# Optimization experiments

Hardware: AMD Instinct MI355X
Metric: run time of the kernel (lower is better)

Reference implementation:

```python
import jax, jax.numpy as jnp
import numpy as np

N, F, O, S, B, E = 100000, 128, 128, 4, 2, 3200000

def setup_inputs() -> dict:
    key = jax.random.key(0)
    k1, k2, k3, k4, k5, k6 = jax.random.split(key, 6)
    features = jax.random.normal(k1, (N, F), dtype=jnp.float32)
    # xavier-ish scale for weights
    W = jax.random.normal(k2, (B, F, O), dtype=jnp.float32) * (1.0 / np.sqrt(F))
    W_comp = jax.random.normal(k3, (S, B), dtype=jnp.float32)
    edge_rows = jax.random.randint(k4, (S, E), 0, N, dtype=jnp.int32)
    edge_cols = jax.random.randint(k5, (S, E), 0, N, dtype=jnp.int32)
    edge_vals = jax.random.uniform(k6, (S, E), dtype=jnp.float32)
    return {"features": features, "W": W, "W_comp": W_comp,
            "edge_rows": edge_rows, "edge_cols": edge_cols, "edge_vals": edge_vals}

def reference(features, W, W_comp, edge_rows, edge_cols, edge_vals):
    # Basis decomposition: V[s] = sum_b W_comp[s,b] * W[b]   -> [S, F, O]
    V = jnp.einsum('sb,bfo->sfo', W_comp, W)
    # supports[s] = features @ V[s]                            -> [S, N, O]
    supports = jnp.einsum('nf,sfo->sno', features, V)
    num_nodes = features.shape[0]
    def agg(sup, rows, cols, vals):
        # sparse A @ sup: gather source rows, scale by edge val, scatter-add to dest
        msgs = sup[cols] * vals[:, None]          # [E, O]
        return jax.ops.segment_sum(msgs, rows, num_segments=num_nodes)
    outs = jax.vmap(agg)(supports, edge_rows, edge_cols, edge_vals)  # [S, N, O]
    return jnp.tanh(outs.sum(axis=0))
```

## Files before the change

kernel.cpp:

```cpp
#include <hip/hip_runtime.h>
#include <hip/hip_bf16.h>
#include <hip/hip_fp16.h>

#define NN 100000
#define FF 128
#define OO 128
#define SS 4
#define BBASES 2
#define EE 3200000
#define TOTE (SS * EE)
#define BROWS 32
#define NBUK 3125
#define NCOARSE 98
#define SCAP 5120
#define RBLOCKS 512
#define P2PARTS 8

typedef unsigned int uintx2 __attribute__((ext_vector_type(2)));
typedef float floatx4 __attribute__((ext_vector_type(4)));

static __device__ __forceinline__ float2 h2_to_f2(unsigned int u) {
  __half2 h = *reinterpret_cast<__half2*>(&u);
  return __half22float2(h);
}


__global__ __launch_bounds__(256) void histB_kernel(
    const int* __restrict__ rows, unsigned int* __restrict__ bhist) {
  __shared__ unsigned int lh[NBUK];
  for (int i = threadIdx.x; i < NBUK; i += 256) lh[i] = 0;
  __syncthreads();
  const int stride = gridDim.x * 256;
  for (int i = blockIdx.x * 256 + threadIdx.x; i < TOTE; i += stride)
    atomicAdd(&lh[((unsigned)rows[i]) >> 5], 1u);
  __syncthreads();
  for (int i = threadIdx.x; i < NBUK; i += 256) {
    unsigned int c = lh[i];
    if (c) atomicAdd(&bhist[i], c);
  }
}

__global__ __launch_bounds__(256) void scanB_kernel(
    const unsigned int* __restrict__ bhist, unsigned int* __restrict__ bstart,
    unsigned int* __restrict__ fcur, unsigned int* __restrict__ ccur) {
  __shared__ unsigned int sums[256];
  const int C = (NBUK + 255) / 256;
  const int t = threadIdx.x;
  unsigned int s = 0;
  for (int j = 0; j < C; ++j) {
    int i = t * C + j;
    if (i < NBUK) s += bhist[i];
  }
  sums[t] = s;
  __syncthreads();
  for (int off = 1; off < 256; off <<= 1) {
    unsigned int v = (t >= off) ? sums[t - off] : 0u;
    __syncthreads();
    sums[t] += v;
    __syncthreads();
  }
  unsigned int base = (t == 0) ? 0u : sums[t - 1];
  for (int j = 0; j < C; ++j) {
    int i = t * C + j;
    if (i < NBUK) {
      unsigned int h = bhist[i];
      bstart[i] = base;
      fcur[i] = base;
      base += h;
    }
  }
  if (t == 255) bstart[NBUK] = base;
  __syncthreads();
  if (t < NCOARSE) ccur[t] = bstart[t * 32];
}

__global__ __launch_bounds__(256) void part1_kernel(
    const int* __restrict__ rows, const int* __restrict__ cols,
    const float* __restrict__ vals, const float* __restrict__ Wc,
    unsigned int* __restrict__ ccur, uintx2* __restrict__ recsA) {
  __shared__ unsigned int lcnt[NCOARSE];
  __shared__ unsigned int lbase[NCOARSE];
  const float c00 = Wc[0], c01 = Wc[1], c10 = Wc[2], c11 = Wc[3];
  const float c20 = Wc[4], c21 = Wc[5], c30 = Wc[6], c31 = Wc[7];
  const int C = (TOTE + RBLOCKS - 1) / RBLOCKS;
  const int start = blockIdx.x * C;
  const int end = min(start + C, TOTE);
  const int tid = threadIdx.x;
  if (tid < NCOARSE) lcnt[tid] = 0;
  __syncthreads();
  for (int i = start + tid; i < end; i += 256)
    atomicAdd(&lcnt[((unsigned)rows[i]) >> 10], 1u);
  __syncthreads();
  if (tid < NCOARSE) {
    unsigned int c = lcnt[tid];
    lbase[tid] = c ? atomicAdd(&ccur[tid], c) : 0u;
    lcnt[tid] = 0;
  }
  __syncthreads();
  for (int i = start + tid; i < end; i += 256) {
    unsigned int r = (unsigned)rows[i];
    int bk = r >> 10;
    unsigned int p = lbase[bk] + atomicAdd(&lcnt[bk], 1u);
    unsigned int s = (unsigned)(i / EE);
    float val = vals[i];
    float w0 = (s == 0) ? c00 : (s == 1) ? c10 : (s == 2) ? c20 : c30;
    float w1 = (s == 0) ? c01 : (s == 1) ? c11 : (s == 2) ? c21 : c31;
    __half2 hv = __floats2half2_rn(val * w0, val * w1);
    uintx2 rec;
    rec.x = ((unsigned)cols[i]) | ((r & 31u) << 17) | (((r >> 5) & 31u) << 22);
    rec.y = *reinterpret_cast<unsigned int*>(&hv);
    recsA[p] = rec;
  }
}

__global__ __launch_bounds__(256) void part2_kernel(
    const uintx2* __restrict__ recsA, const unsigned int* __restrict__ bstart,
    unsigned int* __restrict__ fcur, uintx2* __restrict__ recsB) {
  __shared__ unsigned int lcnt[32];
  __shared__ unsigned int lbase[32];
  const int c = blockIdx.x >> 3;
  const int p = blockIdx.x & (P2PARTS - 1);
  const int f0 = c * 32;
  const int f1 = min(f0 + 32, NBUK);
  const unsigned int beg = bstart[f0];
  const unsigned int endc = bstart[f1];
  const unsigned int len = endc - beg;
  const unsigned int chunk = (len + P2PARTS - 1) / P2PARTS;
  const unsigned int s0 = beg + (unsigned)p * chunk;
  const unsigned int s1 = min(s0 + chunk, endc);
  const int tid = threadIdx.x;
  if (tid < 32) lcnt[tid] = 0;
  __syncthreads();
  for (unsigned int i = s0 + tid; i < s1; i += 256)
    atomicAdd(&lcnt[(recsA[i].x >> 22) & 31u], 1u);
  __syncthreads();
  if (tid < 32) {
    unsigned int cnt = lcnt[tid];
    lbase[tid] = (cnt && f0 + tid < NBUK) ? atomicAdd(&fcur[f0 + tid], cnt) : 0u;
    lcnt[tid] = 0;
  }
  __syncthreads();
  for (unsigned int i = s0 + tid; i < s1; i += 256) {
    uintx2 r = recsA[i];
    unsigned int j = (r.x >> 22) & 31u;
    unsigned int pos = lbase[j] + atomicAdd(&lcnt[j], 1u);
    recsB[pos] = r;
  }
}

#define RBLOCKSB 256
__global__ __launch_bounds__(1024) void partitionB_kernel(
    const int* __restrict__ rows, const int* __restrict__ cols,
    const float* __restrict__ vals, const float* __restrict__ Wc,
    unsigned int* __restrict__ fcur, uintx2* __restrict__ recs) {
  __shared__ unsigned int lcnt[NBUK];
  __shared__ unsigned int lbase[NBUK];
  const float c00 = Wc[0], c01 = Wc[1], c10 = Wc[2], c11 = Wc[3];
  const float c20 = Wc[4], c21 = Wc[5], c30 = Wc[6], c31 = Wc[7];
  const int C = (TOTE + RBLOCKSB - 1) / RBLOCKSB;
  const int start = blockIdx.x * C;
  const int end = min(start + C, TOTE);
  const int tid = threadIdx.x;
  for (int i = tid; i < NBUK; i += 1024) lcnt[i] = 0;
  __syncthreads();
  for (int i = start + tid; i < end; i += 1024)
    atomicAdd(&lcnt[((unsigned)rows[i]) >> 5], 1u);
  __syncthreads();
  for (int i = tid; i < NBUK; i += 1024) {
    unsigned int c = lcnt[i];
    if (c) lbase[i] = atomicAdd(&fcur[i], c);
    lcnt[i] = 0;
  }
  __syncthreads();
  for (int i = start + tid; i < end; i += 1024) {
    unsigned int r = (unsigned)rows[i];
    int bk = r >> 5;
    unsigned int p = lbase[bk] + atomicAdd(&lcnt[bk], 1u);
    unsigned int s = (unsigned)(i / EE);
    float val = vals[i];
    float w0 = (s == 0) ? c00 : (s == 1) ? c10 : (s == 2) ? c20 : c30;
    float w1 = (s == 0) ? c01 : (s == 1) ? c11 : (s == 2) ? c21 : c31;
    __half2 hv = __floats2half2_rn(val * w0, val * w1);
    uintx2 rec;
    rec.x = ((unsigned)cols[i]) | ((r & 31u) << 17) | (((r >> 5) & 31u) << 22);
    rec.y = *reinterpret_cast<unsigned int*>(&hv);
    recs[p] = rec;
  }
}

__global__ __launch_bounds__(256) void cast_kernel(const float* __restrict__ f,
                                                   unsigned int* __restrict__ fb) {
  int i = blockIdx.x * 256 + threadIdx.x;
  float2 a = reinterpret_cast<const float2*>(f)[i];
  __half2 h = __floats2half2_rn(a.x, a.y);
  fb[i] = *reinterpret_cast<unsigned int*>(&h);
}

#define LITERS ((SCAP + 511) / 512)
__global__ __launch_bounds__(512, 8) void pullsort_fused_kernel(
    const unsigned int* __restrict__ featb, const float* __restrict__ W,
    const uintx2* __restrict__ recs, const unsigned int* __restrict__ bstart,
    float* __restrict__ out) {
  __shared__ __align__(16) unsigned char smem[SCAP * 8];
  __shared__ unsigned int h[BROWS], st[BROWS], cur[BROWS];
  uintx2* buf = (uintx2*)smem;
  float* G = (float*)smem;
  const int tid = threadIdx.x;
  const int b = blockIdx.x;
  const unsigned int e0 = bstart[b];
  const unsigned int e1b = bstart[b + 1];
  const int len = (int)(e1b - e0);
  const bool fits = (len <= SCAP);

  if (tid < BROWS) h[tid] = 0;
  __syncthreads();

  uintx2 loc[LITERS];
  if (fits) {
#pragma unroll
    for (int it = 0; it < LITERS; ++it) {
      int i = tid + it * 512;
      if (i < len) {
        uintx2 r = __builtin_nontemporal_load(&recs[e0 + i]);
        loc[it] = r;
        atomicAdd(&h[(r.x >> 17) & 31u], 1u);
      }
    }
  }
  __syncthreads();
  if (tid == 0) {
    unsigned int run = 0;
#pragma unroll
    for (int j = 0; j < BROWS; ++j) {
      st[j] = run;
      cur[j] = run;
      run += h[j];
    }
  }
  __syncthreads();
  if (fits) {
#pragma unroll
    for (int it = 0; it < LITERS; ++it) {
      int i = tid + it * 512;
      if (i < len) {
        uintx2 r = loc[it];
        unsigned int pos = atomicAdd(&cur[(r.x >> 17) & 31u], 1u);
        buf[pos] = r;
      }
    }
  }
  __syncthreads();

  const int nl = tid >> 4;
  const int q = tid & 15;
  float a0[8], a1[8];
#pragma unroll
  for (int k = 0; k < 8; ++k) {
    a0[k] = 0.f;
    a1[k] = 0.f;
  }

  if (fits) {
    const unsigned int rbeg = st[nl];
    const unsigned int rend = rbeg + h[nl];
    for (unsigned int e = rbeg; e < rend; ++e) {
      uintx2 rec = buf[e];
      unsigned int c = rec.x & 0x1FFFFu;
      float2 vv = h2_to_f2(rec.y);
      uint4 xv = *reinterpret_cast<const uint4*>(&featb[(c << 6) + (q << 2)]);
      const __half2* hp = reinterpret_cast<const __half2*>(&xv);
#pragma unroll
      for (int m = 0; m < 4; ++m) {
        float2 f = __half22float2(hp[m]);
        a0[2 * m] += vv.x * f.x;
        a0[2 * m + 1] += vv.x * f.y;
        a1[2 * m] += vv.y * f.x;
        a1[2 * m + 1] += vv.y * f.y;
      }
    }
  } else {
    for (unsigned int e = e0; e < e1b; ++e) {
      uintx2 rec = recs[e];
      if ((int)((rec.x >> 17) & 31u) == nl) {
        unsigned int c = rec.x & 0x1FFFFu;
        float2 vv = h2_to_f2(rec.y);
        uint4 xv = *reinterpret_cast<const uint4*>(&featb[(c << 6) + (q << 2)]);
        const __half2* hp = reinterpret_cast<const __half2*>(&xv);
#pragma unroll
        for (int m = 0; m < 4; ++m) {
          float2 f = __half22float2(hp[m]);
          a0[2 * m] += vv.x * f.x;
          a0[2 * m + 1] += vv.x * f.y;
          a1[2 * m] += vv.y * f.x;
          a1[2 * m + 1] += vv.y * f.y;
        }
      }
    }
  }
  __syncthreads();

#pragma unroll
  for (int k = 0; k < 8; ++k) {
    G[nl * 256 + q * 8 + k] = a0[k];
    G[nl * 256 + FF + q * 8 + k] = a1[k];
  }
  __syncthreads();

  const int tx = tid & 31;
  const int ty = tid >> 5;
  float acc[2][4];
#pragma unroll
  for (int r = 0; r < 2; ++r)
#pragma unroll
    for (int c = 0; c < 4; ++c) acc[r][c] = 0.f;

  for (int k = 0; k < 2 * FF; ++k) {
    float4 bv = *reinterpret_cast<const float4*>(&W[k * OO + tx * 4]);
#pragma unroll
    for (int r = 0; r < 2; ++r) {
      float a = G[(ty * 2 + r) * 256 + k];
      acc[r][0] += a * bv.x;
      acc[r][1] += a * bv.y;
      acc[r][2] += a * bv.z;
      acc[r][3] += a * bv.w;
    }
  }
#pragma unroll
  for (int r = 0; r < 2; ++r) {
    int row = b * BROWS + ty * 2 + r;
    floatx4 o;
    o.x = tanhf(acc[r][0]);
    o.y = tanhf(acc[r][1]);
    o.z = tanhf(acc[r][2]);
    o.w = tanhf(acc[r][3]);
    __builtin_nontemporal_store(o, (floatx4*)&out[(size_t)row * OO + tx * 4]);
  }
}

__global__ void compute_V_kernel(const float* __restrict__ W,
                                 const float* __restrict__ Wc,
                                 float* __restrict__ V) {
  int i = blockIdx.x * blockDim.x + threadIdx.x;
  int s = i >> 14;
  int fo = i & 16383;
  V[i] = Wc[s * BBASES + 0] * W[fo] + Wc[s * BBASES + 1] * W[16384 + fo];
}

__global__ __launch_bounds__(256) void scatter_kernel(
    const float* __restrict__ feat, const int* __restrict__ rows,
    const int* __restrict__ cols, const float* __restrict__ vals,
    float* __restrict__ agg) {
  int t = blockIdx.x * blockDim.x + threadIdx.x;
  int e = t >> 5;
  int qq = t & 31;
  if (e >= EE) return;
  int r = rows[e];
  int c = cols[e];
  float v = vals[e];
  const float4 x = *reinterpret_cast<const float4*>(&feat[(size_t)c * FF + qq * 4]);
  float* dst = &agg[(size_t)r * FF + qq * 4];
  unsafeAtomicAdd(dst + 0, v * x.x);
  unsafeAtomicAdd(dst + 1, v * x.y);
  unsafeAtomicAdd(dst + 2, v * x.z);
  unsafeAtomicAdd(dst + 3, v * x.w);
}

__global__ __launch_bounds__(256) void gemm_acc_kernel(
    const float* __restrict__ A, const float* __restrict__ Bv,
    float* __restrict__ C) {
  __shared__ float As[16][64];
  __shared__ float Bs[16][128];
  const int tid = threadIdx.x;
  const int bm0 = blockIdx.x * 64;
  const int tx = tid & 31;
  const int ty = tid >> 5;
  float acc[8][4];
#pragma unroll
  for (int r = 0; r < 8; ++r)
#pragma unroll
    for (int c = 0; c < 4; ++c) acc[r][c] = 0.0f;
  const int ar = tid >> 2;
  const int akq = tid & 3;
  for (int k0 = 0; k0 < FF; k0 += 16) {
    {
      int row = bm0 + ar;
      float4 av = make_float4(0.f, 0.f, 0.f, 0.f);
      if (row < NN)
        av = *reinterpret_cast<const float4*>(&A[(size_t)row * FF + k0 + akq * 4]);
      As[akq * 4 + 0][ar] = av.x;
      As[akq * 4 + 1][ar] = av.y;
      As[akq * 4 + 2][ar] = av.z;
      As[akq * 4 + 3][ar] = av.w;
    }
#pragma unroll
    for (int i = 0; i < 2; ++i) {
      int v = tid + i * 256;
      int kk = v >> 5;
      int cq = v & 31;
      *reinterpret_cast<float4*>(&Bs[kk][cq * 4]) =
          *reinterpret_cast<const float4*>(&Bv[(k0 + kk) * OO + cq * 4]);
    }
    __syncthreads();
#pragma unroll
    for (int kk = 0; kk < 16; ++kk) {
      float4 b = *reinterpret_cast<const float4*>(&Bs[kk][tx * 4]);
#pragma unroll
      for (int r = 0; r < 8; ++r) {
        float a = As[kk][ty * 8 + r];
        acc[r][0] += a * b.x;
        acc[r][1] += a * b.y;
        acc[r][2] += a * b.z;
        acc[r][3] += a * b.w;
      }
    }
    __syncthreads();
  }
#pragma unroll
  for (int r = 0; r < 8; ++r) {
    int row = bm0 + ty * 8 + r;
    if (row < NN) {
      float4* cp = reinterpret_cast<float4*>(&C[(size_t)row * OO + tx * 4]);
      float4 c = *cp;
      c.x += acc[r][0];
      c.y += acc[r][1];
      c.z += acc[r][2];
      c.w += acc[r][3];
      *cp = c;
    }
  }
}

__global__ __launch_bounds__(256) void tanh_kernel(float* __restrict__ out) {
  int i = blockIdx.x * blockDim.x + threadIdx.x;
  float4* p = reinterpret_cast<float4*>(out) + i;
  float4 v = *p;
  v.x = tanhf(v.x);
  v.y = tanhf(v.y);
  v.z = tanhf(v.z);
  v.w = tanhf(v.w);
  *p = v;
}

extern "C" void kernel_launch(void* const* d_in, const int* in_sizes, int n_in,
                              void* d_out, int out_size, void* d_ws,
                              size_t ws_size, hipStream_t stream) {
  const float* feat = (const float*)d_in[0];
  const float* W = (const float*)d_in[1];
  const float* Wc = (const float*)d_in[2];
  const int* erows = (const int*)d_in[3];
  const int* ecols = (const int*)d_in[4];
  const float* evals = (const float*)d_in[5];
  float* out = (float*)d_out;

  unsigned char* ws = (unsigned char*)d_ws;
  size_t off = 0;
  unsigned int* bhist = (unsigned int*)(ws + off);
  off += (((size_t)NBUK * 4) + 255) & ~(size_t)255;
  unsigned int* bstart = (unsigned int*)(ws + off);
  off += (((size_t)(NBUK + 1) * 4) + 255) & ~(size_t)255;
  unsigned int* fcur = (unsigned int*)(ws + off);
  off += (((size_t)NBUK * 4) + 255) & ~(size_t)255;
  unsigned int* ccur = (unsigned int*)(ws + off);
  off += (((size_t)NCOARSE * 4) + 255) & ~(size_t)255;
  uintx2* recsA = (uintx2*)(ws + off);
  off += (size_t)TOTE * 8;
  unsigned int* featb = (unsigned int*)(ws + off);
  size_t needB = off + (size_t)NN * FF * 2;
  uintx2* recsB = (uintx2*)(ws + needB);
  size_t needA = needB + (size_t)TOTE * 8;

  if (ws_size >= needB) {
    hipMemsetAsync(bhist, 0, (size_t)NBUK * 4, stream);
    histB_kernel<<<RBLOCKS, 256, 0, stream>>>(erows, bhist);
    scanB_kernel<<<1, 256, 0, stream>>>(bhist, bstart, fcur, ccur);
    cast_kernel<<<(NN * FF / 2) / 256, 256, 0, stream>>>(feat, featb);
    if (ws_size >= needA) {
      part1_kernel<<<RBLOCKS, 256, 0, stream>>>(erows, ecols, evals, Wc, ccur,
                                                recsA);
      part2_kernel<<<NCOARSE * P2PARTS, 256, 0, stream>>>(recsA, bstart, fcur,
                                                          recsB);
      pullsort_fused_kernel<<<NBUK, 512, 0, stream>>>(featb, W, recsB, bstart,
                                                      out);
    } else {
      partitionB_kernel<<<RBLOCKSB, 1024, 0, stream>>>(erows, ecols, evals, Wc,
                                                       fcur, recsA);
      pullsort_fused_kernel<<<NBUK, 512, 0, stream>>>(featb, W, recsA, bstart,
                                                      out);
    }
  } else {
    float* V = (float*)d_ws;
    float* agg = V + (size_t)SS * FF * OO;
    compute_V_kernel<<<(SS * FF * OO) / 256, 256, 0, stream>>>(W, Wc, V);
    hipMemsetAsync(out, 0, (size_t)NN * OO * sizeof(float), stream);
    for (int s = 0; s < SS; ++s) {
      hipMemsetAsync(agg, 0, (size_t)NN * FF * sizeof(float), stream);
      scatter_kernel<<<(EE * 32) / 256, 256, 0, stream>>>(
          feat, erows + (size_t)s * EE, ecols + (size_t)s * EE,
          evals + (size_t)s * EE, agg);
      gemm_acc_kernel<<<(NN + 63) / 64, 256, 0, stream>>>(
          agg, V + (size_t)s * FF * OO, out);
    }
    tanh_kernel<<<(NN * OO / 4) / 256, 256, 0, stream>>>(out);
  }
}
```

Before: 772.8 us.

## Use fp16 MFMA for per-bucket dense projection with swizzled LDS tile

Replaces the scalar FP32 FMA loop that multiplied the aggregated 32x256 tile by W with MFMA 16x16x32 fp16 instructions. A new kernel pre-casts W to a transposed fp16 copy, and the aggregated tile is stored in LDS as fp16 with an XOR swizzle to avoid bank conflicts. SCAP is reduced, which lowers LDS use but sends more buckets down the overflow path. Rounding the accumulated features to fp16 before the matmul adds precision loss and a risk of overflow.

```diff
diff --git a/kernel.cpp b/kernel.cpp
--- a/kernel.cpp
+++ b/kernel.cpp
@@ -12,12 +12,14 @@
 #define BROWS 32
 #define NBUK 3125
 #define NCOARSE 98
-#define SCAP 5120
+#define SCAP 4608
 #define RBLOCKS 512
 #define P2PARTS 8
 
 typedef unsigned int uintx2 __attribute__((ext_vector_type(2)));
 typedef float floatx4 __attribute__((ext_vector_type(4)));
+typedef _Float16 f16x8 __attribute__((ext_vector_type(8)));
+typedef float f32x4 __attribute__((ext_vector_type(4)));
 
 static __device__ __forceinline__ float2 h2_to_f2(unsigned int u) {
   __half2 h = *reinterpret_cast<__half2*>(&u);
@@ -196,15 +198,23 @@
   fb[i] = *reinterpret_cast<unsigned int*>(&h);
 }
 
+__global__ __launch_bounds__(256) void castW_kernel(const float* __restrict__ W,
+                                                    _Float16* __restrict__ Wt) {
+  int i = blockIdx.x * 256 + threadIdx.x;
+  int o = i & (OO - 1);
+  int k = i >> 7;
+  Wt[(size_t)o * (2 * FF) + k] = (_Float16)W[i];
+}
+
 #define LITERS ((SCAP + 511) / 512)
 __global__ __launch_bounds__(512, 8) void pullsort_fused_kernel(
-    const unsigned int* __restrict__ featb, const float* __restrict__ W,
+    const unsigned int* __restrict__ featb, const _Float16* __restrict__ Wt,
     const uintx2* __restrict__ recs, const unsigned int* __restrict__ bstart,
     float* __restrict__ out) {
   __shared__ __align__(16) unsigned char smem[SCAP * 8];
   __shared__ unsigned int h[BROWS], st[BROWS], cur[BROWS];
   uintx2* buf = (uintx2*)smem;
-  float* G = (float*)smem;
+  _Float16* G_h = (_Float16*)smem;
   const int tid = threadIdx.x;
   const int b = blockIdx.x;
   const unsigned int e0 = bstart[b];
@@ -299,41 +309,49 @@
   }
   __syncthreads();
 
-#pragma unroll
-  for (int k = 0; k < 8; ++k) {
-    G[nl * 256 + q * 8 + k] = a0[k];
-    G[nl * 256 + FF + q * 8 + k] = a1[k];
-  }
-  __syncthreads();
-
-  const int tx = tid & 31;
-  const int ty = tid >> 5;
-  float acc[2][4];
-#pragma unroll
-  for (int r = 0; r < 2; ++r)
-#pragma unroll
-    for (int c = 0; c < 4; ++c) acc[r][c] = 0.f;
-
-  for (int k = 0; k < 2 * FF; ++k) {
-    float4 bv = *reinterpret_cast<const float4*>(&W[k * OO + tx * 4]);
-#pragma unroll
-    for (int r = 0; r < 2; ++r) {
-      float a = G[(ty * 2 + r) * 256 + k];
-      acc[r][0] += a * bv.x;
-      acc[r][1] += a * bv.y;
-      acc[r][2] += a * bv.z;
-      acc[r][3] += a * bv.w;
-    }
-  }
-#pragma unroll
-  for (int r = 0; r < 2; ++r) {
-    int row = b * BROWS + ty * 2 + r;
-    floatx4 o;
-    o.x = tanhf(acc[r][0]);
-    o.y = tanhf(acc[r][1]);
-    o.z = tanhf(acc[r][2]);
-    o.w = tanhf(acc[r][3]);
-    __builtin_nontemporal_store(o, (floatx4*)&out[(size_t)row * OO + tx * 4]);
+  {
+    f16x8 h0, h1;
+#pragma unroll
+    for (int k = 0; k < 8; ++k) {
+      h0[k] = (_Float16)a0[k];
+      h1[k] = (_Float16)a1[k];
+    }
+    int g0 = q ^ (nl & 7);
+    int g1 = (16 + q) ^ (nl & 7);
+    *reinterpret_cast<f16x8*>(&G_h[nl * 256 + g0 * 8]) = h0;
+    *reinterpret_cast<f16x8*>(&G_h[nl * 256 + g1 * 8]) = h1;
+  }
+  __syncthreads();
+
+  const int wv = tid >> 6;
+  const int lane = tid & 63;
+  const int m = wv & 1;
+  const int n0 = wv >> 1;
+  const int arow = m * 16 + (lane & 15);
+  const int gsel = lane >> 4;
+  f32x4 acc0 = {0.f, 0.f, 0.f, 0.f};
+  f32x4 acc1 = {0.f, 0.f, 0.f, 0.f};
+#pragma unroll
+  for (int kk = 0; kk < 8; ++kk) {
+    int gr = kk * 4 + gsel;
+    f16x8 af = *reinterpret_cast<const f16x8*>(
+        &G_h[arow * 256 + (gr ^ (arow & 7)) * 8]);
+    int kbase = kk * 32 + gsel * 8;
+    f16x8 b0 = *reinterpret_cast<const f16x8*>(
+        &Wt[(size_t)(n0 * 16 + (lane & 15)) * 256 + kbase]);
+    f16x8 b1 = *reinterpret_cast<const f16x8*>(
+        &Wt[(size_t)((n0 + 4) * 16 + (lane & 15)) * 256 + kbase]);
+    acc0 = __builtin_amdgcn_mfma_f32_16x16x32_f16(af, b0, acc0, 0, 0, 0);
+    acc1 = __builtin_amdgcn_mfma_f32_16x16x32_f16(af, b1, acc1, 0, 0, 0);
+  }
+  {
+    int crow = b * BROWS + m * 16 + (lane >> 4) * 4;
+    int ccol = lane & 15;
+#pragma unroll
+    for (int r = 0; r < 4; ++r) {
+      out[(size_t)(crow + r) * OO + n0 * 16 + ccol] = tanhf(acc0[r]);
+      out[(size_t)(crow + r) * OO + (n0 + 4) * 16 + ccol] = tanhf(acc1[r]);
+    }
   }
 }
 
@@ -465,7 +483,9 @@
   uintx2* recsA = (uintx2*)(ws + off);
   off += (size_t)TOTE * 8;
   unsigned int* featb = (unsigned int*)(ws + off);
-  size_t needB = off + (size_t)NN * FF * 2;
+  off += (size_t)NN * FF * 2;
+  _Float16* Wt = (_Float16*)(ws + off);
+  size_t needB = off + (size_t)2 * FF * OO * 2;
   uintx2* recsB = (uintx2*)(ws + needB);
   size_t needA = needB + (size_t)TOTE * 8;
 
@@ -474,17 +494,18 @@
     histB_kernel<<<RBLOCKS, 256, 0, stream>>>(erows, bhist);
     scanB_kernel<<<1, 256, 0, stream>>>(bhist, bstart, fcur, ccur);
     cast_kernel<<<(NN * FF / 2) / 256, 256, 0, stream>>>(feat, featb);
+    castW_kernel<<<(2 * FF * OO) / 256, 256, 0, stream>>>(W, Wt);
     if (ws_size >= needA) {
       part1_kernel<<<RBLOCKS, 256, 0, stream>>>(erows, ecols, evals, Wc, ccur,
                                                 recsA);
       part2_kernel<<<NCOARSE * P2PARTS, 256, 0, stream>>>(recsA, bstart, fcur,
                                                           recsB);
-      pullsort_fused_kernel<<<NBUK, 512, 0, stream>>>(featb, W, recsB, bstart,
+      pullsort_fused_kernel<<<NBUK, 512, 0, stream>>>(featb, Wt, recsB, bstart,
                                                       out);
     } else {
       partitionB_kernel<<<RBLOCKSB, 1024, 0, stream>>>(erows, ecols, evals, Wc,
                                                        fcur, recsA);
-      pullsort_fused_kernel<<<NBUK, 512, 0, stream>>>(featb, W, recsA, bstart,
+      pullsort_fused_kernel<<<NBUK, 512, 0, stream>>>(featb, Wt, recsA, bstart,
                                                       out);
     }
   } else {
```

Measured after the change: 718.8 us. -7.0%, faster.
